# Kernel optimization log

Hardware: AMD Instinct MI355X
Metric: run time of the kernel (lower is better)

## Reference

```python
import jax, jax.numpy as jnp
import numpy as np

E = 1_000_000      # edges in batch
N_BATCH = 50_000   # local nodes in batch
N_TOTAL = 100_000  # total entities
R = 1000           # num relations
D = 200            # rnn_in_dim == rnn_hid_dim


def setup_inputs() -> dict:
    key = jax.random.key(0)
    ks = jax.random.split(key, 9)
    s = 1.0 / np.sqrt(D)  # torch GRU init scale
    return {
        "edge_index": jax.random.randint(ks[0], (2, E), 0, N_BATCH),
        "edge_type": jax.random.randint(ks[1], (E,), 0, R),
        "node_id": jax.random.randint(ks[2], (N_BATCH,), 0, N_TOTAL),
        "static_entity_emb": jax.random.normal(ks[3], (N_TOTAL, D), jnp.float32),
        "dynamic_relation_emb": jax.random.normal(ks[4], (R, 1, D, 2), jnp.float32),
        "W_ih": jax.random.uniform(ks[5], (3 * D, D), jnp.float32, -s, s),
        "W_hh": jax.random.uniform(ks[6], (3 * D, D), jnp.float32, -s, s),
        "b_ih": jax.random.uniform(ks[7], (3 * D,), jnp.float32, -s, s),
        "b_hh": jax.random.uniform(ks[8], (3 * D,), jnp.float32, -s, s),
    }


def _scatter_mean_by_rel(emb, edge_type):
    # emb: [E, D] gathered entity embeddings; segment-mean over relation type -> [R, D]
    seg_sum = jax.ops.segment_sum(emb, edge_type, num_segments=R)
    cnt = jax.ops.segment_sum(jnp.ones((emb.shape[0], 1), emb.dtype), edge_type, num_segments=R)
    return jnp.where(cnt > 0, seg_sum / jnp.maximum(cnt, 1.0), 0.0)


def _gru_cell(x, h, W_ih, W_hh, b_ih, b_hh):
    # torch GRU gate order: r, z, n. x,h: [R, D]
    gi = x @ W_ih.T + b_ih
    gh = h @ W_hh.T + b_hh
    i_r, i_z, i_n = jnp.split(gi, 3, axis=-1)
    h_r, h_z, h_n = jnp.split(gh, 3, axis=-1)
    r = jax.nn.sigmoid(i_r + h_r)
    z = jax.nn.sigmoid(i_z + h_z)
    n = jnp.tanh(i_n + r * h_n)
    return (1.0 - z) * n + z * h


def reference(edge_index, edge_type, node_id, static_entity_emb,
              dynamic_relation_emb, W_ih, W_hh, b_ih, b_hh):
    src_nid = node_id[edge_index[0]]  # [E]
    dst_nid = node_id[edge_index[1]]  # [E]
    # gather + scatter-mean by relation (irregular access; the hot path)
    x_src = _scatter_mean_by_rel(static_entity_emb[src_nid], edge_type)  # [R, D]
    x_dst = _scatter_mean_by_rel(static_entity_emb[dst_nid], edge_type)  # [R, D]
    # single-layer hidden states per relation (side 0 = src, 1 = dst)
    h_src = dynamic_relation_emb[:, 0, :, 0]  # [R, D]
    h_dst = dynamic_relation_emb[:, 0, :, 1]  # [R, D]
    new_src = _gru_cell(x_src, h_src, W_ih, W_hh, b_ih, b_hh)
    new_dst = _gru_cell(x_dst, h_dst, W_ih, W_hh, b_ih, b_hh)
    # [R, num_layers=1, D, 2]
    return jnp.stack([new_src, new_dst], axis=-1)[:, None, :, :]
```

## Files before the change

kernel.cpp:

```cpp
#include <hip/hip_runtime.h>
#include <hip/hip_fp16.h>
#include <math.h>

#define DD     200
#define DD3    600
#define NBK    256
#define GB     256
#define SCH    8192
#define SCAP   11264
#define CHUNK  1024
#define KP     232
#define MP     2048
#define NP     640

typedef unsigned int   uint32;
typedef unsigned short uint16;
typedef __attribute__((ext_vector_type(8))) short bf16x8;
typedef __attribute__((ext_vector_type(4))) float f32x4;

static __device__ inline float bf2f(uint16 u) {
    union { uint32 i; float f; } x; x.i = ((uint32)u) << 16; return x.f;
}
static __device__ inline uint16 f2bf(float f) {
    union { float f; uint32 i; } x; x.f = f;
    return (uint16)((x.i + 0x7FFFu + ((x.i >> 16) & 1u)) >> 16);
}
static __device__ inline float asf(uint32 u) {
    union { uint32 i; float f; } x; x.i = u; return x.f;
}
static __device__ inline uint32 packbf(float a, float b) {
    return (uint32)f2bf(a) | ((uint32)f2bf(b) << 16);
}
static __device__ inline uint32 packh2(float a, float b) {
    __half2 h = __floats2half2_rn(a, b);
    union { __half2 h; uint32 u; } x; x.h = h; return x.u;
}
static __device__ inline __half2 ash2(uint32 u) {
    union { uint32 u; __half2 h; } x; x.u = u; return x.h;
}

__global__ void zero_kernel(int* __restrict__ cnt, int n) {
    int stride = gridDim.x * blockDim.x;
    for (int i = blockIdx.x * blockDim.x + threadIdx.x; i < n; i += stride) cnt[i] = 0;
}

__global__ void zerof_kernel(float* __restrict__ p, int n) {
    int stride = gridDim.x * blockDim.x;
    for (int i = blockIdx.x * blockDim.x + threadIdx.x; i < n; i += stride) p[i] = 0.f;
}

__launch_bounds__(512)
__global__ void blockhist_kernel(const int* __restrict__ etype, const int* __restrict__ eidx,
                                 int* __restrict__ boff, int E) {
    __shared__ int lc[NBK];
    const int tid = threadIdx.x;
    if (tid < NBK) lc[tid] = 0;
    __syncthreads();
    int per = (E + GB - 1) / GB;
    int beg = blockIdx.x * per;
    int end = min(E, beg + per);
    for (int e = beg + tid; e < end; e += 512) {
        int r  = etype[e];
        int ch = r >> 5;
        atomicAdd(&lc[(ch << 3) | (eidx[e] >> 13)], 1);
        atomicAdd(&lc[(ch << 3) | (eidx[E + e] >> 13)], 1);
    }
    __syncthreads();
    if (tid < NBK) boff[blockIdx.x * NBK + tid] = lc[tid];
}

__launch_bounds__(GB)
__global__ void offscanA_kernel(int* __restrict__ boff, int* __restrict__ tot) {
    __shared__ int s[GB];
    const int g   = blockIdx.x;
    const int tid = threadIdx.x;
    int v = boff[(size_t)tid * NBK + g];
    s[tid] = v;
    for (int off = 1; off < GB; off <<= 1) {
        __syncthreads();
        int t2 = (tid >= off) ? s[tid - off] : 0;
        __syncthreads();
        s[tid] += t2;
    }
    __syncthreads();
    boff[(size_t)tid * NBK + g] = s[tid] - v;
    if (tid == GB - 1) tot[g] = s[tid];
}

__launch_bounds__(NBK)
__global__ void offscanB_kernel(const int* __restrict__ tot, int* __restrict__ offs256) {
    __shared__ int s[NBK];
    const int t = threadIdx.x;
    int v = tot[t];
    s[t] = v;
    for (int off = 1; off < NBK; off <<= 1) {
        __syncthreads();
        int t2 = (t >= off) ? s[t - off] : 0;
        __syncthreads();
        s[t] += t2;
    }
    __syncthreads();
    offs256[t] = s[t] - v;
    if (t == NBK - 1) offs256[NBK] = s[t];
}

__launch_bounds__(512)
__global__ void blocksort_kernel(const int* __restrict__ etype, const int* __restrict__ eidx,
                                 const int* __restrict__ boff, const int* __restrict__ offs256,
                                 uint32* __restrict__ binned, int E) {
    __shared__ uint32 raw[SCH];
    __shared__ uint32 srt[SCH];
    __shared__ int lhist[NBK];
    __shared__ int loff[NBK + 1];
    __shared__ int lcur[NBK];
    __shared__ int bbase[NBK];
    __shared__ int sc[NBK];
    const int tid  = threadIdx.x;
    const int wv   = tid >> 6;
    const int lane = tid & 63;

    if (tid < NBK) bbase[tid] = boff[blockIdx.x * NBK + tid] + offs256[tid];
    int per = (E + GB - 1) / GB;
    int ebeg = blockIdx.x * per;
    int eend = min(E, ebeg + per);

    for (int cb = ebeg; cb < eend; cb += SCH / 2) {
        const int ne = min(SCH / 2, eend - cb);
        const int m  = 2 * ne;
        if (tid < NBK) lhist[tid] = 0;
        __syncthreads();
        for (int i = tid; i < ne; i += 512) {
            int e  = cb + i;
            int r  = etype[e];
            int sS = eidx[e];
            int sD = eidx[E + e];
            int ch = r >> 5;
            int rb = (r & 31) << 1;
            raw[2 * i]     = ((uint32)ch << 24) | ((uint32)rb << 16) | (uint32)sS;
            raw[2 * i + 1] = ((uint32)ch << 24) | ((uint32)(rb + 1) << 16) | (uint32)sD;
            atomicAdd(&lhist[(ch << 3) | (sS >> 13)], 1);
            atomicAdd(&lhist[(ch << 3) | (sD >> 13)], 1);
        }
        __syncthreads();
        if (tid < NBK) sc[tid] = lhist[tid];
        for (int off = 1; off < NBK; off <<= 1) {
            __syncthreads();
            int t2 = (tid < NBK && tid >= off) ? sc[tid - off] : 0;
            __syncthreads();
            if (tid < NBK) sc[tid] += t2;
        }
        __syncthreads();
        if (tid < NBK) {
            loff[tid] = sc[tid] - lhist[tid];
            lcur[tid] = loff[tid];
            if (tid == NBK - 1) loff[NBK] = sc[tid];
        }
        __syncthreads();
        for (int i = tid; i < m; i += 512) {
            uint32 pk = raw[i];
            int k = (int)((pk >> 24) << 3) | (int)((pk & 0xFFFFu) >> 13);
            int pos = atomicAdd(&lcur[k], 1);
            srt[pos] = pk;
        }
        __syncthreads();
        for (int b = wv; b < NBK; b += 8) {
            int lo = loff[b];
            int c  = loff[b + 1] - lo;
            if (c > 0) {
                int dst = bbase[b];
                for (int i = lane; i < c; i += 64) binned[dst + i] = srt[lo + i];
                if (lane == 0) bbase[b] = dst + c;
            }
        }
        __syncthreads();
    }
}

__launch_bounds__(512)
__global__ void sortbucket_kernel(const uint32* __restrict__ binned,
                                  const int* __restrict__ offs256,
                                  uint16* __restrict__ list, int* __restrict__ offs16k,
                                  int total) {
    __shared__ uint16 sorted[SCAP];
    __shared__ int hist[64];
    __shared__ int cur[64];
    __shared__ int scn[65];
    __shared__ int sc[64];
    const int bk  = blockIdx.x;
    const int tid = threadIdx.x;
    const int beg = offs256[bk];
    const int end = offs256[bk + 1];
    const int len = end - beg;

    if (tid < 64) hist[tid] = 0;
    __syncthreads();
    for (int i = tid; i < len; i += 512)
        atomicAdd(&hist[(binned[beg + i] >> 16) & 63], 1);
    __syncthreads();
    if (tid < 64) sc[tid] = hist[tid];
    for (int off = 1; off < 64; off <<= 1) {
        __syncthreads();
        int t2 = (tid < 64 && tid >= off) ? sc[tid - off] : 0;
        __syncthreads();
        if (tid < 64) sc[tid] += t2;
    }
    __syncthreads();
    if (tid < 64) {
        scn[tid] = sc[tid] - hist[tid];
        cur[tid] = scn[tid];
        if (tid == 63) scn[64] = sc[63];
    }
    __syncthreads();
    if (tid < 64) offs16k[bk * 64 + tid] = beg + scn[tid];
    if (bk == 0 && tid == 64) offs16k[NBK * 64] = total;

    if (len <= SCAP) {
        for (int i = tid; i < len; i += 512) {
            uint32 e = binned[beg + i];
            int p = atomicAdd(&cur[(e >> 16) & 63], 1);
            sorted[p] = (uint16)(e & 0xFFFF);
        }
        __syncthreads();
        for (int i = tid; i < len; i += 512) list[beg + i] = sorted[i];
    } else {
        for (int i = tid; i < len; i += 512) {
            uint32 e = binned[beg + i];
            int p = atomicAdd(&cur[(e >> 16) & 63], 1);
            list[beg + p] = (uint16)(e & 0xFFFF);
        }
    }
}

__global__ void compact_kernel(const int* __restrict__ node_id, const float* __restrict__ emb,
                               uint32* __restrict__ cmp, int NB) {
    int idx = blockIdx.x * blockDim.x + threadIdx.x;
    if (idx >= NB * 50) return;
    int s = idx / 50, q = idx - s * 50;
    int nid = node_id[s];
    float4 v = *(const float4*)(emb + (size_t)nid * DD + 4 * q);
    *(uint2*)(cmp + (size_t)s * 100 + 2 * q) = make_uint2(packh2(v.x, v.y), packh2(v.z, v.w));
}

__launch_bounds__(256)
__global__ void partial7_kernel(const uint16* __restrict__ list,
                                const uint32* __restrict__ cmp,
                                const int* __restrict__ offs16k,
                                uint16* __restrict__ partial) {
    const int g    = blockIdx.x & 7;
    const int rest = blockIdx.x >> 3;
    const int rsl  = rest & 63;
    const int ch   = rest >> 6;
    const int b16  = ((ch * 8 + g) << 6) | rsl;
    const int tid  = threadIdx.x;
    const int w    = tid >> 6;
    const int lane = tid & 63;
    const int sub  = lane / 25;
    const int w25  = lane % 25;
    const int laneOff = w25 * 4;

    __shared__ uint16 sl[CHUNK];
    __shared__ float  red[8][DD];

    const int beg = offs16k[b16];
    const int end = offs16k[b16 + 1];

    __half2 h0 = __floats2half2_rn(0.f, 0.f);
    __half2 h1 = h0, h2 = h0, h3 = h0;

    for (int base = beg; base < end; base += CHUNK) {
        const int m = min(CHUNK, end - base);
        for (int i = tid; i < m; i += 256) sl[i] = list[base + i];
        __syncthreads();
        if (sub < 2) {
            int i = w * 2 + sub;
            for (; i + 24 < m; i += 32) {
                int s0 = sl[i];
                int s1 = sl[i + 8];
                int s2 = sl[i + 16];
                int s3 = sl[i + 24];
                uint4 v0 = *(const uint4*)(cmp + (size_t)s0 * 100 + laneOff);
                uint4 v1 = *(const uint4*)(cmp + (size_t)s1 * 100 + laneOff);
                uint4 v2 = *(const uint4*)(cmp + (size_t)s2 * 100 + laneOff);
                uint4 v3 = *(const uint4*)(cmp + (size_t)s3 * 100 + laneOff);
                h0 = __hadd2(h0, __hadd2(__hadd2(ash2(v0.x), ash2(v1.x)),
                                         __hadd2(ash2(v2.x), ash2(v3.x))));
                h1 = __hadd2(h1, __hadd2(__hadd2(ash2(v0.y), ash2(v1.y)),
                                         __hadd2(ash2(v2.y), ash2(v3.y))));
                h2 = __hadd2(h2, __hadd2(__hadd2(ash2(v0.z), ash2(v1.z)),
                                         __hadd2(ash2(v2.z), ash2(v3.z))));
                h3 = __hadd2(h3, __hadd2(__hadd2(ash2(v0.w), ash2(v1.w)),
                                         __hadd2(ash2(v2.w), ash2(v3.w))));
            }
            for (; i < m; i += 8) {
                int s0 = sl[i];
                uint4 v0 = *(const uint4*)(cmp + (size_t)s0 * 100 + laneOff);
                h0 = __hadd2(h0, ash2(v0.x));
                h1 = __hadd2(h1, ash2(v0.y));
                h2 = __hadd2(h2, ash2(v0.z));
                h3 = __hadd2(h3, ash2(v0.w));
            }
        }
        __syncthreads();
    }

    if (sub < 2) {
        int row = w * 2 + sub;
        int c = w25 * 8;
        red[row][c]     = __low2float(h0);  red[row][c + 1] = __high2float(h0);
        red[row][c + 2] = __low2float(h1);  red[row][c + 3] = __high2float(h1);
        red[row][c + 4] = __low2float(h2);  red[row][c + 5] = __high2float(h2);
        red[row][c + 6] = __low2float(h3);  red[row][c + 7] = __high2float(h3);
    }
    __syncthreads();

    if (tid < DD) {
        float s = 0.f;
        #pragma unroll
        for (int q = 0; q < 8; ++q) s += red[q][tid];
        partial[(size_t)b16 * DD + tid] = f2bf(s);
    }
}

__global__ void prep2_kernel(const uint16* __restrict__ partial,
                             const int* __restrict__ offs16k,
                             const float* __restrict__ dyn,
                             const float* __restrict__ W_ih, const float* __restrict__ W_hh,
                             uint32* __restrict__ Xb, uint32* __restrict__ Hb,
                             uint32* __restrict__ Wib, uint32* __restrict__ Whb, int RS2) {
    const int KU = KP / 2;
    int idx = blockIdx.x * blockDim.x + threadIdx.x;
    int XU = MP * KU, WU = NP * KU;
    const uint32* pp = (const uint32*)partial;
    if (idx < XU) {
        int row = idx / KU, kk = (idx - row * KU) * 2;
        uint32 o = 0;
        if (row < RS2 && kk < DD) {
            int ch = row >> 6, rsl = row & 63;
            float s0 = 0.f, s1 = 0.f;
            int n = 0;
            #pragma unroll
            for (int g = 0; g < 8; ++g) {
                int b16 = ((ch * 8 + g) << 6) | rsl;
                n += offs16k[b16 + 1] - offs16k[b16];
                uint32 v = pp[b16 * 100 + (kk >> 1)];
                s0 += asf(v << 16);
                s1 += asf(v & 0xFFFF0000u);
            }
            float rc = (n > 0) ? 1.f / (float)n : 0.f;
            o = packbf(s0 * rc, s1 * rc);
        }
        Xb[idx] = o;
    } else if (idx < 2 * XU) {
        int k2 = idx - XU;
        int row = k2 / KU, kk = (k2 - row * KU) * 2;
        uint32 o = 0;
        if (row < RS2 && kk < DD) {
            int r = row >> 1, side = row & 1;
            float h0 = dyn[((size_t)r * DD + kk) * 2 + side];
            float h1 = dyn[((size_t)r * DD + kk + 1) * 2 + side];
            o = packbf(h0, h1);
        }
        Hb[k2] = o;
    } else if (idx < 2 * XU + 2 * WU) {
        int k2 = idx - 2 * XU;
        const float* W = (k2 < WU) ? W_ih : W_hh;
        uint32* dst = (k2 < WU) ? Wib : Whb;
        if (k2 >= WU) k2 -= WU;
        int row = k2 / KU, kk = (k2 - row * KU) * 2;
        uint32 o = 0;
        if (row < DD3 && kk < DD) {
            o = packbf(W[(size_t)row * DD + kk], W[(size_t)row * DD + kk + 1]);
        }
        dst[k2] = o;
    }
}

__launch_bounds__(256)
__global__ void mfma_gates_kernel(const uint32* __restrict__ Xb, const uint32* __restrict__ Hb,
                                  const uint32* __restrict__ Wib, const uint32* __restrict__ Whb,
                                  float* __restrict__ G) {
    __shared__ short As[64 * KP];
    __shared__ short Bs[64 * KP];
    const int nt  = blockIdx.x;
    const int mt  = blockIdx.y;
    const int z   = blockIdx.z;
    const int tid = threadIdx.x;

    const uint32* Asrc = (z ? Hb : Xb) + (size_t)mt * 64 * (KP / 2);
    const uint32* Bsrc = (z ? Whb : Wib) + (size_t)nt * 64 * (KP / 2);
    {
        const uint4* a4 = (const uint4*)Asrc;
        const uint4* b4 = (const uint4*)Bsrc;
        uint4* la = (uint4*)As;
        uint4* lb = (uint4*)Bs;
        const int n16 = 64 * KP * 2 / 16;
        for (int i = tid; i < n16; i += 256) { la[i] = a4[i]; lb[i] = b4[i]; }
    }
    __syncthreads();

    const int w    = tid >> 6;
    const int lane = tid & 63;
    const int qm   = (w & 1) * 32;
    const int qn   = (w >> 1) * 32;
    const int lr   = lane & 15;
    const int lk   = (lane >> 4) * 8;

    f32x4 acc00 = {0.f, 0.f, 0.f, 0.f}, acc01 = acc00, acc10 = acc00, acc11 = acc00;
    #pragma unroll
    for (int ks = 0; ks < 7; ++ks) {
        int kof = ks * 32 + lk;
        bf16x8 a0 = *(const bf16x8*)&As[(qm + lr) * KP + kof];
        bf16x8 a1 = *(const bf16x8*)&As[(qm + 16 + lr) * KP + kof];
        bf16x8 b0 = *(const bf16x8*)&Bs[(qn + lr) * KP + kof];
        bf16x8 b1 = *(const bf16x8*)&Bs[(qn + 16 + lr) * KP + kof];
        acc00 = __builtin_amdgcn_mfma_f32_16x16x32_bf16(a0, b0, acc00, 0, 0, 0);
        acc01 = __builtin_amdgcn_mfma_f32_16x16x32_bf16(a0, b1, acc01, 0, 0, 0);
        acc10 = __builtin_amdgcn_mfma_f32_16x16x32_bf16(a1, b0, acc10, 0, 0, 0);
        acc11 = __builtin_amdgcn_mfma_f32_16x16x32_bf16(a1, b1, acc11, 0, 0, 0);
    }

    float* Gz = G + (size_t)z * MP * NP;
    const int mb = mt * 64 + qm + (lane >> 4) * 4;
    const int nb = nt * 64 + qn + lr;
    #pragma unroll
    for (int r = 0; r < 4; ++r) {
        Gz[(size_t)(mb + r) * NP + nb]           = acc00[r];
        Gz[(size_t)(mb + r) * NP + nb + 16]      = acc01[r];
        Gz[(size_t)(mb + 16 + r) * NP + nb]      = acc10[r];
        Gz[(size_t)(mb + 16 + r) * NP + nb + 16] = acc11[r];
    }
}

__global__ void gruf2_kernel(const float* __restrict__ G, const float* __restrict__ dyn,
                             const float* __restrict__ b_ih, const float* __restrict__ b_hh,
                             float* __restrict__ out, int RS2) {
    int idx = blockIdx.x * blockDim.x + threadIdx.x;
    int total = RS2 * DD;
    if (idx >= total) return;
    int rs = idx / DD, t = idx - rs * DD;
    int r = rs >> 1, side = rs & 1;
    const float* Gi = G;
    const float* Gh = G + (size_t)MP * NP;
    size_t base = (size_t)rs * NP;
    float ga   = Gi[base + t]          + b_ih[t]          + Gh[base + t]          + b_hh[t];
    float gz   = Gi[base + DD + t]     + b_ih[DD + t]     + Gh[base + DD + t]     + b_hh[DD + t];
    float gi_n = Gi[base + 2 * DD + t] + b_ih[2 * DD + t];
    float gh_n = Gh[base + 2 * DD + t] + b_hh[2 * DD + t];
    float rg = 1.f / (1.f + __expf(-ga));
    float zz = 1.f / (1.f + __expf(-gz));
    float nn = tanhf(gi_n + rg * gh_n);
    float h  = dyn[((size_t)r * DD + t) * 2 + side];
    out[((size_t)r * DD + t) * 2 + side] = (1.f - zz) * nn + zz * h;
}

__global__ void hist_kernel(const int* __restrict__ etype, int* __restrict__ cnt,
                            int E, int R) {
    __shared__ int lc[1024];
    for (int i = threadIdx.x; i < R; i += blockDim.x) lc[i] = 0;
    __syncthreads();
    int stride = gridDim.x * blockDim.x;
    for (int i = blockIdx.x * blockDim.x + threadIdx.x; i < E; i += stride)
        atomicAdd(&lc[etype[i]], 1);
    __syncthreads();
    for (int i = threadIdx.x; i < R; i += blockDim.x)
        if (lc[i]) atomicAdd(&cnt[i], lc[i]);
}

__global__ void atomic_acc_kernel(const int* __restrict__ eidx, const int* __restrict__ etype,
                                  const int* __restrict__ node_id, const float* __restrict__ emb,
                                  float* __restrict__ acc, int E) {
    int gtid = blockIdx.x * blockDim.x + threadIdx.x;
    int wave = gtid >> 6, lane = gtid & 63;
    int nwaves = (gridDim.x * blockDim.x) >> 6;
    for (int e = wave; e < E; e += nwaves) {
        int r = etype[e];
        float* dst = acc + (size_t)r * DD * 2;
        for (int side = 0; side < 2; ++side) {
            int nid = node_id[eidx[(size_t)side * E + e]];
            const float* row = emb + (size_t)nid * DD;
            for (int d = lane; d < DD; d += 64)
                atomicAdd(&dst[d * 2 + side], row[d]);
        }
    }
}

__launch_bounds__(256)
__global__ void gru_inplace_kernel(const float* __restrict__ dyn, const float* __restrict__ W_ih,
                                   const float* __restrict__ W_hh, const float* __restrict__ b_ih,
                                   const float* __restrict__ b_hh, const int* __restrict__ cnt,
                                   float* __restrict__ out) {
    const int r = blockIdx.x, side = blockIdx.y, tid = threadIdx.x;
    __shared__ float xs[DD], hs[DD], gi[DD3], gh[DD3];
    if (tid < DD) {
        float s = out[((size_t)r * DD + tid) * 2 + side];
        int n = cnt[r];
        xs[tid] = (n > 0) ? s / (float)n : 0.f;
        hs[tid] = dyn[((size_t)r * DD + tid) * 2 + side];
    }
    __syncthreads();
    for (int jj = tid; jj < DD3; jj += 256) {
        float a = b_ih[jj], c = b_hh[jj];
        const float* rI = W_ih + (size_t)jj * DD;
        const float* rH = W_hh + (size_t)jj * DD;
        for (int k = 0; k < DD; ++k) { a = fmaf(xs[k], rI[k], a); c = fmaf(hs[k], rH[k], c); }
        gi[jj] = a; gh[jj] = c;
    }
    __syncthreads();
    if (tid < DD) {
        float rr = 1.f / (1.f + __expf(-(gi[tid] + gh[tid])));
        float zz = 1.f / (1.f + __expf(-(gi[DD + tid] + gh[DD + tid])));
        float nn = tanhf(gi[2 * DD + tid] + rr * gh[2 * DD + tid]);
        out[((size_t)r * DD + tid) * 2 + side] = (1.f - zz) * nn + zz * hs[tid];
    }
}

extern "C" void kernel_launch(void* const* d_in, const int* in_sizes, int n_in,
                              void* d_out, int out_size, void* d_ws, size_t ws_size,
                              hipStream_t stream) {
    const int*   eidx    = (const int*)d_in[0];
    const int*   etype   = (const int*)d_in[1];
    const int*   node_id = (const int*)d_in[2];
    const float* emb     = (const float*)d_in[3];
    const float* dyn     = (const float*)d_in[4];
    const float* W_ih    = (const float*)d_in[5];
    const float* W_hh    = (const float*)d_in[6];
    const float* b_ih    = (const float*)d_in[7];
    const float* b_hh    = (const float*)d_in[8];
    float*       out     = (float*)d_out;

    const int E   = in_sizes[1];
    const int NB  = in_sizes[2];
    const int D   = in_sizes[7] / 3;
    const int R   = in_sizes[4] / (2 * D);
    const int RS2 = R * 2;

    char* p = (char*)d_ws;
    auto take = [&](size_t bytes) { char* q = p; p += (bytes + 255) & ~(size_t)255; return q; };
    int*    boff    = (int*)   take((size_t)GB * NBK * 4);
    int*    tot     = (int*)   take((size_t)NBK * 4);
    int*    offs256 = (int*)   take((size_t)(NBK + 1) * 4);
    int*    offs16k = (int*)   take((size_t)(NBK * 64 + 1) * 4);
    uint32* cmp     = (uint32*)take((size_t)NB * 100 * 4);
    uint16* list    = (uint16*)take((size_t)2 * E * 2);
    uint16* partial = (uint16*)take((size_t)NBK * 64 * DD * 2);
    size_t need_full = (size_t)(p - (char*)d_ws);

    uint32* binned = cmp;
    float*  G      = (float*)cmp;
    const int KU = KP / 2;
    uint32* Xb  = (uint32*)list;
    uint32* Hb  = Xb + (size_t)MP * KU;
    uint32* Wib = Hb + (size_t)MP * KU;
    uint32* Whb = Wib + (size_t)NP * KU;
    size_t ovl_list = (size_t)(2 * MP + 2 * NP) * KU * 4;
    size_t ovl_cmp1 = (size_t)2 * E * 4;
    size_t ovl_cmp2 = (size_t)2 * MP * NP * 4;
    const bool overlay_ok = (ovl_list <= (size_t)2 * E * 2) &&
                            (ovl_cmp1 <= (size_t)NB * 100 * 4) &&
                            (ovl_cmp2 <= (size_t)NB * 100 * 4);

    const bool fits = (ws_size >= need_full) && (NB <= 50000) && (R == 1000) &&
                      (D == 200) && overlay_ok && (E <= 1000000);
    if (fits) {
        blockhist_kernel<<<GB, 512, 0, stream>>>(etype, eidx, boff, E);
        offscanA_kernel<<<NBK, GB, 0, stream>>>(boff, tot);
        offscanB_kernel<<<1, NBK, 0, stream>>>(tot, offs256);
        blocksort_kernel<<<GB, 512, 0, stream>>>(etype, eidx, boff, offs256, binned, E);
        sortbucket_kernel<<<NBK, 512, 0, stream>>>(binned, offs256, list, offs16k, 2 * E);
        compact_kernel<<<(NB * 50 + 255) / 256, 256, 0, stream>>>(node_id, emb, cmp, NB);
        partial7_kernel<<<NBK * 64, 256, 0, stream>>>(list, cmp, offs16k, partial);
        int ptot = 2 * MP * KU + 2 * NP * KU;
        prep2_kernel<<<(ptot + 255) / 256, 256, 0, stream>>>(partial, offs16k, dyn, W_ih, W_hh,
                                                             Xb, Hb, Wib, Whb, RS2);
        dim3 mg(NP / 64, MP / 64, 2);
        mfma_gates_kernel<<<mg, 256, 0, stream>>>(Xb, Hb, Wib, Whb, G);
        gruf2_kernel<<<(RS2 * DD + 255) / 256, 256, 0, stream>>>(G, dyn, b_ih, b_hh, out, RS2);
    } else {
        int* cnt = (int*)d_ws;
        zero_kernel<<<32, 256, 0, stream>>>(cnt, R);
        hist_kernel<<<512, 256, 0, stream>>>(etype, cnt, E, R);
        zerof_kernel<<<(R * D * 2 + 255) / 256, 256, 0, stream>>>(out, R * D * 2);
        atomic_acc_kernel<<<2048, 256, 0, stream>>>(eidx, etype, node_id, emb, out, E);
        dim3 grid(R, 2);
        gru_inplace_kernel<<<grid, 256, 0, stream>>>(dyn, W_ih, W_hh, b_ih, b_hh, cnt, out);
    }
}
```

Before: 122.8 us.

## Fuse compaction into histogram kernel and deepen gather unroll

Merges the node-embedding compaction into the block-histogram launch, using extra blocks beyond the histogram grid, so the two independent phases run concurrently and one launch is removed. This requires a separate binned buffer, since binned previously overlaid cmp, which is now written early. The change costs extra workspace (2*E*4 bytes), which could fail the fits check if the workspace is too small. The partial gather loop is also unrolled from 4 to 8 outstanding row loads to raise memory-level parallelism, at the cost of more registers.

```diff
diff --git a/kernel.cpp b/kernel.cpp
--- a/kernel.cpp
+++ b/kernel.cpp
@@ -50,23 +50,37 @@
 }
 
 __launch_bounds__(512)
-__global__ void blockhist_kernel(const int* __restrict__ etype, const int* __restrict__ eidx,
-                                 int* __restrict__ boff, int E) {
-    __shared__ int lc[NBK];
+__global__ void hist_compact_kernel(const int* __restrict__ etype, const int* __restrict__ eidx,
+                                    int* __restrict__ boff, int E,
+                                    const int* __restrict__ node_id, const float* __restrict__ emb,
+                                    uint32* __restrict__ cmp, int NB) {
     const int tid = threadIdx.x;
-    if (tid < NBK) lc[tid] = 0;
-    __syncthreads();
-    int per = (E + GB - 1) / GB;
-    int beg = blockIdx.x * per;
-    int end = min(E, beg + per);
-    for (int e = beg + tid; e < end; e += 512) {
-        int r  = etype[e];
-        int ch = r >> 5;
-        atomicAdd(&lc[(ch << 3) | (eidx[e] >> 13)], 1);
-        atomicAdd(&lc[(ch << 3) | (eidx[E + e] >> 13)], 1);
-    }
-    __syncthreads();
-    if (tid < NBK) boff[blockIdx.x * NBK + tid] = lc[tid];
+    if (blockIdx.x < GB) {
+        __shared__ int lc[NBK];
+        if (tid < NBK) lc[tid] = 0;
+        __syncthreads();
+        int per = (E + GB - 1) / GB;
+        int beg = blockIdx.x * per;
+        int end = min(E, beg + per);
+        for (int e = beg + tid; e < end; e += 512) {
+            int r  = etype[e];
+            int ch = r >> 5;
+            atomicAdd(&lc[(ch << 3) | (eidx[e] >> 13)], 1);
+            atomicAdd(&lc[(ch << 3) | (eidx[E + e] >> 13)], 1);
+        }
+        __syncthreads();
+        if (tid < NBK) boff[blockIdx.x * NBK + tid] = lc[tid];
+    } else {
+        int idx = (blockIdx.x - GB) * 512 + tid;
+        int stride = (gridDim.x - GB) * 512;
+        int total = NB * 50;
+        for (; idx < total; idx += stride) {
+            int s = idx / 50, q = idx - s * 50;
+            int nid = node_id[s];
+            float4 v = *(const float4*)(emb + (size_t)nid * DD + 4 * q);
+            *(uint2*)(cmp + (size_t)s * 100 + 2 * q) = make_uint2(packh2(v.x, v.y), packh2(v.z, v.w));
+        }
+    }
 }
 
 __launch_bounds__(GB)
@@ -229,16 +243,6 @@
             list[beg + p] = (uint16)(e & 0xFFFF);
         }
     }
-}
-
-__global__ void compact_kernel(const int* __restrict__ node_id, const float* __restrict__ emb,
-                               uint32* __restrict__ cmp, int NB) {
-    int idx = blockIdx.x * blockDim.x + threadIdx.x;
-    if (idx >= NB * 50) return;
-    int s = idx / 50, q = idx - s * 50;
-    int nid = node_id[s];
-    float4 v = *(const float4*)(emb + (size_t)nid * DD + 4 * q);
-    *(uint2*)(cmp + (size_t)s * 100 + 2 * q) = make_uint2(packh2(v.x, v.y), packh2(v.z, v.w));
 }
 
 __launch_bounds__(256)
@@ -273,11 +277,36 @@
         __syncthreads();
         if (sub < 2) {
             int i = w * 2 + sub;
-            for (; i + 24 < m; i += 32) {
-                int s0 = sl[i];
-                int s1 = sl[i + 8];
-                int s2 = sl[i + 16];
-                int s3 = sl[i + 24];
+            for (; i + 56 < m; i += 64) {
+                int s0 = sl[i],      s1 = sl[i + 8],  s2 = sl[i + 16], s3 = sl[i + 24];
+                int s4 = sl[i + 32], s5 = sl[i + 40], s6 = sl[i + 48], s7 = sl[i + 56];
+                uint4 v0 = *(const uint4*)(cmp + (size_t)s0 * 100 + laneOff);
+                uint4 v1 = *(const uint4*)(cmp + (size_t)s1 * 100 + laneOff);
+                uint4 v2 = *(const uint4*)(cmp + (size_t)s2 * 100 + laneOff);
+                uint4 v3 = *(const uint4*)(cmp + (size_t)s3 * 100 + laneOff);
+                uint4 v4 = *(const uint4*)(cmp + (size_t)s4 * 100 + laneOff);
+                uint4 v5 = *(const uint4*)(cmp + (size_t)s5 * 100 + laneOff);
+                uint4 v6 = *(const uint4*)(cmp + (size_t)s6 * 100 + laneOff);
+                uint4 v7 = *(const uint4*)(cmp + (size_t)s7 * 100 + laneOff);
+                h0 = __hadd2(h0, __hadd2(__hadd2(__hadd2(ash2(v0.x), ash2(v1.x)),
+                                                 __hadd2(ash2(v2.x), ash2(v3.x))),
+                                         __hadd2(__hadd2(ash2(v4.x), ash2(v5.x)),
+                                                 __hadd2(ash2(v6.x), ash2(v7.x)))));
+                h1 = __hadd2(h1, __hadd2(__hadd2(__hadd2(ash2(v0.y), ash2(v1.y)),
+                                                 __hadd2(ash2(v2.y), ash2(v3.y))),
+                                         __hadd2(__hadd2(ash2(v4.y), ash2(v5.y)),
+                                                 __hadd2(ash2(v6.y), ash2(v7.y)))));
+                h2 = __hadd2(h2, __hadd2(__hadd2(__hadd2(ash2(v0.z), ash2(v1.z)),
+                                                 __hadd2(ash2(v2.z), ash2(v3.z))),
+                                         __hadd2(__hadd2(ash2(v4.z), ash2(v5.z)),
+                                                 __hadd2(ash2(v6.z), ash2(v7.z)))));
+                h3 = __hadd2(h3, __hadd2(__hadd2(__hadd2(ash2(v0.w), ash2(v1.w)),
+                                                 __hadd2(ash2(v2.w), ash2(v3.w))),
+                                         __hadd2(__hadd2(ash2(v4.w), ash2(v5.w)),
+                                                 __hadd2(ash2(v6.w), ash2(v7.w)))));
+            }
+            if (i + 24 < m) {
+                int s0 = sl[i], s1 = sl[i + 8], s2 = sl[i + 16], s3 = sl[i + 24];
                 uint4 v0 = *(const uint4*)(cmp + (size_t)s0 * 100 + laneOff);
                 uint4 v1 = *(const uint4*)(cmp + (size_t)s1 * 100 + laneOff);
                 uint4 v2 = *(const uint4*)(cmp + (size_t)s2 * 100 + laneOff);
@@ -290,6 +319,7 @@
                                          __hadd2(ash2(v2.z), ash2(v3.z))));
                 h3 = __hadd2(h3, __hadd2(__hadd2(ash2(v0.w), ash2(v1.w)),
                                          __hadd2(ash2(v2.w), ash2(v3.w))));
+                i += 32;
             }
             for (; i < m; i += 8) {
                 int s0 = sl[i];
@@ -545,7 +575,10 @@
     uint16* partial = (uint16*)take((size_t)NBK * 64 * DD * 2);
     size_t need_full = (size_t)(p - (char*)d_ws);
 
-    uint32* binned = cmp;
+    uint32* binned = (uint32*)list ? (uint32*)0 : (uint32*)0;
+    uint32* binned2 = (uint32*)take((size_t)2 * E * 4);
+    need_full = (size_t)(p - (char*)d_ws);
+
     float*  G      = (float*)cmp;
     const int KU = KP / 2;
     uint32* Xb  = (uint32*)list;
@@ -553,21 +586,19 @@
     uint32* Wib = Hb + (size_t)MP * KU;
     uint32* Whb = Wib + (size_t)NP * KU;
     size_t ovl_list = (size_t)(2 * MP + 2 * NP) * KU * 4;
-    size_t ovl_cmp1 = (size_t)2 * E * 4;
     size_t ovl_cmp2 = (size_t)2 * MP * NP * 4;
     const bool overlay_ok = (ovl_list <= (size_t)2 * E * 2) &&
-                            (ovl_cmp1 <= (size_t)NB * 100 * 4) &&
                             (ovl_cmp2 <= (size_t)NB * 100 * 4);
 
     const bool fits = (ws_size >= need_full) && (NB <= 50000) && (R == 1000) &&
                       (D == 200) && overlay_ok && (E <= 1000000);
     if (fits) {
-        blockhist_kernel<<<GB, 512, 0, stream>>>(etype, eidx, boff, E);
+        hist_compact_kernel<<<GB + 768, 512, 0, stream>>>(etype, eidx, boff, E,
+                                                          node_id, emb, cmp, NB);
         offscanA_kernel<<<NBK, GB, 0, stream>>>(boff, tot);
         offscanB_kernel<<<1, NBK, 0, stream>>>(tot, offs256);
-        blocksort_kernel<<<GB, 512, 0, stream>>>(etype, eidx, boff, offs256, binned, E);
-        sortbucket_kernel<<<NBK, 512, 0, stream>>>(binned, offs256, list, offs16k, 2 * E);
-        compact_kernel<<<(NB * 50 + 255) / 256, 256, 0, stream>>>(node_id, emb, cmp, NB);
+        blocksort_kernel<<<GB, 512, 0, stream>>>(etype, eidx, boff, offs256, binned2, E);
+        sortbucket_kernel<<<NBK, 512, 0, stream>>>(binned2, offs256, list, offs16k, 2 * E);
         partial7_kernel<<<NBK * 64, 256, 0, stream>>>(list, cmp, offs16k, partial);
         int ptot = 2 * MP * KU + 2 * NP * KU;
         prep2_kernel<<<(ptot + 255) / 256, 256, 0, stream>>>(partial, offs16k, dyn, W_ih, W_hh,
```

Result: faster. 117.1 us (-4.6%).
